# Optimization experiments

Hardware: AMD Instinct MI355X
Metric: run time of the kernel (lower is better)

The kernel has to match this reference:

```python
import jax, jax.numpy as jnp
import numpy as np

N_NODES = 100000
N_HEDGES = 50000
N_INC = 300000
N_GRAPHS = 1024
D_IN = 49
D = 512
L = 3
EPS = 1e-5


def _layernorm(x, g, b):
    mu = jnp.mean(x, axis=-1, keepdims=True)
    var = jnp.var(x, axis=-1, keepdims=True)
    return (x - mu) * jax.lax.rsqrt(var + EPS) * g + b


def setup_inputs() -> dict:
    key = jax.random.key(0)
    ks = jax.random.split(key, 20)
    s = 0.02
    inp = {
        "node_features": jax.random.normal(ks[0], (N_NODES, D_IN), jnp.float32),
        "node_idx": jax.random.randint(ks[1], (N_INC,), 0, N_NODES),
        "hedge_idx": jax.random.randint(ks[2], (N_INC,), 0, N_HEDGES),
        "hyperedge_types": jax.random.randint(ks[3], (N_HEDGES,), 0, 3),
        "batch_indices": jnp.sort(jax.random.randint(ks[4], (N_NODES,), 0, N_GRAPHS)),
        "num_graphs": N_GRAPHS,
        "in_w": jax.random.normal(ks[5], (D_IN, D), jnp.float32) * s,
        "in_b": jnp.zeros((D,), jnp.float32),
        "type_emb": jax.random.normal(ks[6], (3, D), jnp.float32) * s,
        "l1_w": jax.random.normal(ks[7], (L, D, D), jnp.float32) * s,
        "l1_b": jnp.zeros((L, D), jnp.float32),
        "l2_w": jax.random.normal(ks[8], (L, D, D), jnp.float32) * s,
        "l2_b": jnp.zeros((L, D), jnp.float32),
        "ln_g": jnp.ones((L, D), jnp.float32),
        "ln_b": jnp.zeros((L, D), jnp.float32),
        "out_w": jax.random.normal(ks[9], (D, D), jnp.float32) * s,
        "out_b": jnp.zeros((D,), jnp.float32),
    }
    return inp


def reference(node_features, node_idx, hedge_idx, hyperedge_types, batch_indices,
              num_graphs, in_w, in_b, type_emb, l1_w, l1_b, l2_w, l2_b,
              ln_g, ln_b, out_w, out_b):
    n_nodes = node_features.shape[0]
    n_hedges = hyperedge_types.shape[0]
    ones_e = jnp.ones((node_idx.shape[0],), node_features.dtype)
    # degrees are constant across layers
    hedge_deg = jnp.clip(jax.ops.segment_sum(ones_e, hedge_idx, num_segments=n_hedges), 1.0)[:, None]
    node_deg = jnp.clip(jax.ops.segment_sum(ones_e, node_idx, num_segments=n_nodes), 1.0)[:, None]

    x = node_features @ in_w + in_b  # [N, D]
    for i in range(L):
        x_trans = x @ l1_w[i] + l1_b[i]                                        # [N, D]
        hedge_aggr = jax.ops.segment_sum(x_trans[node_idx], hedge_idx,
                                         num_segments=n_hedges)                # [H, D]
        hedge_msg = hedge_aggr / hedge_deg + type_emb[hyperedge_types]         # [H, D]
        node_aggr = jax.ops.segment_sum(hedge_msg[hedge_idx], node_idx,
                                        num_segments=n_nodes) / node_deg       # [N, D]
        out = node_aggr @ l2_w[i] + l2_b[i]
        out = x + out  # in_dim == out_dim -> residual
        x = jax.nn.gelu(_layernorm(out, ln_g[i], ln_b[i]), approximate=False)

    node_embs = x
    graph_sum = jax.ops.segment_sum(x, batch_indices, num_segments=num_graphs)  # [B, D]
    counts = jnp.clip(jax.ops.segment_sum(jnp.ones((n_nodes,), x.dtype),
                                          batch_indices, num_segments=num_graphs), 1.0)[:, None]
    graph_emb = (graph_sum / counts) @ out_w + out_b
    return graph_emb, node_embs, batch_indices
```

## Files before the change

### kernel.cpp

```cpp
#include <hip/hip_runtime.h>
#include <math.h>

#define N_NODES  100000
#define N_HEDGES 50000
#define HPAD     50176
#define N_INC    300000
#define N_GRAPHS 1024
#define D_IN     49
#define D        512
#define NPAD     100096
#define KPAD_IN  64

typedef __attribute__((ext_vector_type(8))) short short8;
typedef __attribute__((ext_vector_type(8))) __bf16 bf16x8;
typedef __attribute__((ext_vector_type(4))) float f32x4;

__device__ __forceinline__ short f2bf(float f) {
    union { float f; unsigned u; } v; v.f = f;
    unsigned r = v.u + 0x7fffu + ((v.u >> 16) & 1u);
    return (short)(r >> 16);
}
__device__ __forceinline__ float bf2f(short s) {
    union { unsigned u; float f; } v; v.u = ((unsigned)(unsigned short)s) << 16;
    return v.f;
}

__device__ __forceinline__ float fast_gelu(float y) {
    const float y2 = y * y;
    const float p  = fmaf(y2, 0.0356774081f, 0.7978845608f);
    float arg = y * p * 2.8853900818f;
    arg = fminf(fmaxf(arg, -30.0f), 30.0f);
    const float u = __builtin_exp2f(arg);
    return y * u * __builtin_amdgcn_rcpf(1.0f + u);
}

__device__ __forceinline__ void gld16(const void* g, void* l) {
    __builtin_amdgcn_global_load_lds(
        (const __attribute__((address_space(1))) unsigned int*)g,
        (__attribute__((address_space(3))) unsigned int*)l, 16, 0, 0);
}

__global__ __launch_bounds__(512) void gemm_bf16(
    const short* __restrict__ A, const short* __restrict__ Bt,
    const float* __restrict__ bias,
    short* __restrict__ Cbf, float* __restrict__ Cf, short* __restrict__ CbfT, int strideT,
    const int* __restrict__ hcnt, const int* __restrict__ htypes,
    const float* __restrict__ tembW2, const float* __restrict__ bb,
    int K, int nby, int layerWGs, long aStr, long bStr, long cStr)
{
    __shared__ short lds[24576];
    const int tid  = threadIdx.x;
    const int lane = tid & 63;
    const int wave = tid >> 6;
    const int wr = wave >> 1;
    const int wc = wave & 1;

    const int nwg = gridDim.x;
    const int q8 = nwg >> 3, r8 = nwg & 7;
    const int xcd = blockIdx.x & 7, loc = blockIdx.x >> 3;
    int wg = (xcd < r8) ? (xcd * (q8 + 1) + loc) : (r8 * (q8 + 1) + (xcd - r8) * q8 + loc);
    if (layerWGs) {
        const int layer = wg / layerWGs;
        wg %= layerWGs;
        A += layer * aStr;
        Bt += layer * bStr;
        if (CbfT) CbfT += layer * cStr;
    }
    const long row0 = (long)(wg / nby) * 256;
    const int  col0 = (wg % nby) * 128;

    f32x4 acc[4][4];
    #pragma unroll
    for (int m = 0; m < 4; m++)
        #pragma unroll
        for (int n = 0; n < 4; n++)
            acc[m][n] = (f32x4)(0.0f);

    const int ch   = lane & 3;
    const int rofs = lane >> 2;
    const short* aSrc[2];
    const short* bSrc;
    #pragma unroll
    for (int j = 0; j < 2; j++) {
        const int rloc = (wave * 2 + j) * 16 + rofs;
        const int sw = (rloc >> 1) & 3;
        aSrc[j] = A + (row0 + rloc) * (long)K + (ch ^ sw) * 8;
    }
    {
        const int rlb = wave * 16 + rofs;
        const int swb = (rlb >> 1) & 3;
        bSrc = Bt + ((long)col0 + rlb) * K + (ch ^ swb) * 8;
    }

    const int ks = lane >> 4;
    const int rl = lane & 15;
    const int nk = K >> 5;

    gld16(aSrc[0], &lds[(wave * 2) * 16 * 32]);
    gld16(aSrc[1], &lds[(wave * 2 + 1) * 16 * 32]);
    gld16(bSrc,    &lds[16384 + wave * 16 * 32]);
    if (nk > 1) {
        gld16(aSrc[0] + 32, &lds[8192 + (wave * 2) * 16 * 32]);
        gld16(aSrc[1] + 32, &lds[8192 + (wave * 2 + 1) * 16 * 32]);
        gld16(bSrc    + 32, &lds[16384 + 4096 + wave * 16 * 32]);
    }

    for (int t = 0; t < nk; t++) {
        if (t + 1 < nk) asm volatile("s_waitcnt vmcnt(3)" ::: "memory");
        else            asm volatile("s_waitcnt vmcnt(0)" ::: "memory");
        __builtin_amdgcn_s_barrier();
        __builtin_amdgcn_sched_barrier(0);
        const int cb = t & 1;
        bf16x8 a[4], b[4];
        #pragma unroll
        for (int m = 0; m < 4; m++) {
            const int rr = wr * 64 + m * 16 + rl;
            a[m] = *(const bf16x8*)&lds[cb * 8192 + rr * 32 + (ks ^ ((rr >> 1) & 3)) * 8];
        }
        #pragma unroll
        for (int n = 0; n < 4; n++) {
            const int rr = wc * 64 + n * 16 + rl;
            b[n] = *(const bf16x8*)&lds[16384 + cb * 4096 + rr * 32 + (ks ^ ((rr >> 1) & 3)) * 8];
        }
        #pragma unroll
        for (int m = 0; m < 4; m++)
            #pragma unroll
            for (int n = 0; n < 4; n++)
                acc[m][n] = __builtin_amdgcn_mfma_f32_16x16x32_bf16(a[m], b[n], acc[m][n], 0, 0, 0);
        __builtin_amdgcn_sched_barrier(0);
        __builtin_amdgcn_s_barrier();
        if (t + 2 < nk) {
            gld16(aSrc[0] + (t + 2) * 32, &lds[cb * 8192 + (wave * 2) * 16 * 32]);
            gld16(aSrc[1] + (t + 2) * 32, &lds[cb * 8192 + (wave * 2 + 1) * 16 * 32]);
            gld16(bSrc    + (t + 2) * 32, &lds[16384 + cb * 4096 + wave * 16 * 32]);
        }
    }

    const int rl2 = lane & 15;
    if (Cbf && !Cf && !CbfT) {
        float bbv[4], tw0[4], tw1[4], tw2[4], biv[4];
        #pragma unroll
        for (int n = 0; n < 4; n++) {
            const int col = col0 + wc * 64 + n * 16 + rl2;
            if (hcnt) {
                bbv[n] = bb[col];
                tw0[n] = tembW2[col];
                tw1[n] = tembW2[D + col];
                tw2[n] = tembW2[2 * D + col];
            } else {
                biv[n] = bias ? bias[col] : 0.0f;
            }
        }
        short* ep = &lds[wave * 2304];
        #pragma unroll
        for (int p = 0; p < 2; p++) {
            #pragma unroll
            for (int mm = 0; mm < 2; mm++) {
                const int m = 2 * p + mm;
                #pragma unroll
                for (int rr = 0; rr < 4; rr++) {
                    const long row = row0 + wr * 64 + m * 16 + (lane >> 4) * 4 + rr;
                    const int  lr  = mm * 16 + (lane >> 4) * 4 + rr;
                    if (hcnt) {
                        const float cf  = (float)hcnt[row];
                        const float icf = 1.0f / fmaxf(cf, 1.0f);
                        const int ty = (row < N_HEDGES) ? htypes[row] : 0;
                        #pragma unroll
                        for (int n = 0; n < 4; n++) {
                            float tsel = (ty == 0) ? tw0[n] : (ty == 1) ? tw1[n] : tw2[n];
                            float v = (acc[m][n][rr] + cf * bbv[n]) * icf + tsel;
                            ep[lr * 72 + n * 16 + rl2] = f2bf(v);
                        }
                    } else {
                        #pragma unroll
                        for (int n = 0; n < 4; n++) {
                            float v = acc[m][n][rr] + biv[n];
                            ep[lr * 72 + n * 16 + rl2] = f2bf(v);
                        }
                    }
                }
            }
            __syncthreads();
            #pragma unroll
            for (int i = 0; i < 4; i++) {
                const int lr2 = i * 8 + (lane >> 3);
                const int c2  = lane & 7;
                short8 vv = *(const short8*)&ep[lr2 * 72 + c2 * 8];
                const long row = row0 + wr * 64 + p * 32 + lr2;
                *(short8*)&Cbf[row * D + col0 + wc * 64 + c2 * 8] = vv;
            }
            __syncthreads();
        }
    } else {
        const int rb4 = wr * 64 + (lane >> 4) * 4;
        #pragma unroll
        for (int m = 0; m < 4; m++) {
            #pragma unroll
            for (int n = 0; n < 4; n++) {
                const int col = col0 + wc * 64 + n * 16 + rl2;
                const float bi = bias ? bias[col] : 0.0f;
                #pragma unroll
                for (int rr = 0; rr < 4; rr++) {
                    const long row = row0 + rb4 + m * 16 + rr;
                    float v = acc[m][n][rr];
                    if (hcnt) {
                        const float cf = (float)hcnt[row];
                        const int ty = (row < N_HEDGES) ? htypes[row] : 0;
                        v = (v + cf * bb[col]) * (1.0f / fmaxf(cf, 1.0f)) + tembW2[(long)ty * D + col];
                    } else {
                        v += bi;
                    }
                    if (Cbf)  Cbf[row * D + col] = f2bf(v);
                    if (Cf)   Cf[row * D + col]  = v;
                    if (CbfT && row < strideT) CbfT[(long)col * strideT + row] = f2bf(v);
                }
            }
        }
    }
}

__global__ void count_inc_kernel(const int* __restrict__ nidx, const int* __restrict__ hidx,
                                 int* cnt_n, int* cnt_h) {
    int i = blockIdx.x * 256 + threadIdx.x;
    if (i < N_INC) {
        atomicAdd(&cnt_h[hidx[i]], 1);
        atomicAdd(&cnt_n[nidx[i]], 1);
    }
}

__global__ __launch_bounds__(256) void scan1_kernel(const int* __restrict__ cnt, int* __restrict__ out,
                                                    int* __restrict__ bsum, int n) {
    __shared__ int s[256];
    const int t = threadIdx.x;
    const long base = (long)blockIdx.x * 2048 + t * 8;
    int v[8];
    int ts = 0;
    #pragma unroll
    for (int j = 0; j < 8; j++) {
        v[j] = (base + j < n) ? cnt[base + j] : 0;
        ts += v[j];
    }
    s[t] = ts;
    __syncthreads();
    for (int ofs = 1; ofs < 256; ofs <<= 1) {
        int x = (t >= ofs) ? s[t - ofs] : 0;
        __syncthreads();
        s[t] += x;
        __syncthreads();
    }
    int run = (t == 0) ? 0 : s[t - 1];
    #pragma unroll
    for (int j = 0; j < 8; j++) {
        if (base + j < n) out[base + j] = run;
        run += v[j];
    }
    if (t == 255) bsum[blockIdx.x] = s[255];
}

__global__ __launch_bounds__(256) void scan2_kernel(int* __restrict__ bsum, int nb, int* __restrict__ total) {
    __shared__ int s[256];
    const int t = threadIdx.x;
    int v = (t < nb) ? bsum[t] : 0;
    s[t] = v;
    __syncthreads();
    for (int ofs = 1; ofs < 256; ofs <<= 1) {
        int x = (t >= ofs) ? s[t - ofs] : 0;
        __syncthreads();
        s[t] += x;
        __syncthreads();
    }
    if (t < nb) bsum[t] = (t == 0) ? 0 : s[t - 1];
    if (t == 255) *total = s[255];
}

__global__ __launch_bounds__(256) void scan3_kernel(int* __restrict__ out, const int* __restrict__ bsum, int n) {
    const int add = bsum[blockIdx.x];
    if (add == 0) return;
    const long base = (long)blockIdx.x * 2048 + threadIdx.x * 8;
    #pragma unroll
    for (int j = 0; j < 8; j++)
        if (base + j < n) out[base + j] += add;
}

__global__ void place_kernel(const int* __restrict__ nidx, const int* __restrict__ hidx,
                             const int* __restrict__ hoff, const int* __restrict__ noff,
                             int* hcur, int* ncur, int* __restrict__ hlist, int* __restrict__ nlist) {
    int e = blockIdx.x * 256 + threadIdx.x;
    if (e < N_INC) {
        int h = hidx[e], n = nidx[e];
        int p = atomicAdd(&hcur[h], 1);
        hlist[hoff[h] + p] = n;
        int q = atomicAdd(&ncur[n], 1);
        nlist[noff[n] + q] = h;
    }
}

__global__ void wtrans_kernel(const float* __restrict__ W, short* __restrict__ Wt, int K, int Kpad) {
    int n = blockIdx.x;
    for (int k = threadIdx.x; k < Kpad; k += 64)
        Wt[(long)n * Kpad + k] = (k < K) ? f2bf(W[(long)k * D + n]) : (short)0;
}

__global__ void wtrans3_kernel(const float* __restrict__ W, short* __restrict__ Wt) {
    int layer = blockIdx.x >> 9;
    int n = blockIdx.x & 511;
    const float* src = W + (size_t)layer * D * D;
    short* dst = Wt + (size_t)layer * D * D;
    for (int k = threadIdx.x; k < D; k += 64)
        dst[(long)n * D + k] = f2bf(src[(long)k * D + n]);
}

__global__ void cvt_f32_bf16_kernel(const float* __restrict__ src, short* __restrict__ dst) {
    long i = ((long)blockIdx.x * 256 + threadIdx.x) * 8;
    float4 f0 = *(const float4*)(src + i);
    float4 f1 = *(const float4*)(src + i + 4);
    short8 o;
    o[0] = f2bf(f0.x); o[1] = f2bf(f0.y); o[2] = f2bf(f0.z); o[3] = f2bf(f0.w);
    o[4] = f2bf(f1.x); o[5] = f2bf(f1.y); o[6] = f2bf(f1.z); o[7] = f2bf(f1.w);
    *(short8*)(dst + i) = o;
}

__global__ void cvt_w_pad_kernel(const float* __restrict__ src, short* __restrict__ dst, int rows_real) {
    int r = blockIdx.x;
    int c = threadIdx.x * 8;
    short8 o = (short8)0;
    if (r < rows_real) {
        float4 f0 = *(const float4*)(src + (long)r * D + c);
        float4 f1 = *(const float4*)(src + (long)r * D + c + 4);
        o[0] = f2bf(f0.x); o[1] = f2bf(f0.y); o[2] = f2bf(f0.z); o[3] = f2bf(f0.w);
        o[4] = f2bf(f1.x); o[5] = f2bf(f1.y); o[6] = f2bf(f1.z); o[7] = f2bf(f1.w);
    }
    *(short8*)(dst + (long)r * D + c) = o;
}

__global__ __launch_bounds__(256) void vecmat_kernel(const float* __restrict__ v,
                                                     const float* __restrict__ M,
                                                     float* __restrict__ out) {
    int col = blockIdx.x * 256 + threadIdx.x;
    float a = 0.f;
    for (int j = 0; j < D; j++) a += v[j] * M[(long)j * D + col];
    out[col] = a;
}

__global__ void vecadd_kernel(const float* __restrict__ a, const float* __restrict__ b,
                              float* __restrict__ o) {
    int i = blockIdx.x * 256 + threadIdx.x;
    o[i] = a[i] + b[i];
}

__global__ __launch_bounds__(256) void smallmm3_kernel(
    const float* __restrict__ temb, const float* __restrict__ l1b,
    const float* __restrict__ l2w, float* __restrict__ TB)
{
    int layer = blockIdx.x >> 1;
    int col = (blockIdx.x & 1) * 256 + threadIdx.x;
    const float* b1 = l1b + (size_t)layer * D;
    const float* W2 = l2w + (size_t)layer * D * D;
    float a0 = 0.f, a1 = 0.f, a2 = 0.f, a3 = 0.f;
    for (int j = 0; j < D; j++) {
        float w = W2[(long)j * D + col];
        a0 += temb[j] * w;
        a1 += temb[D + j] * w;
        a2 += temb[2 * D + j] * w;
        a3 += b1[j] * w;
    }
    float* o = TB + (size_t)layer * 4 * D;
    o[col] = a0; o[D + col] = a1; o[2 * D + col] = a2; o[3 * D + col] = a3;
}

__global__ void cvt_in_kernel(const float* __restrict__ nf, short* __restrict__ A0) {
    int r = blockIdx.x;
    int c = threadIdx.x;
    short v = 0;
    if (r < N_NODES && c < D_IN) v = f2bf(nf[(long)r * D_IN + c]);
    A0[(long)r * KPAD_IN + c] = v;
}

__global__ __launch_bounds__(256) void hedge_sum_kernel(
    const short* __restrict__ x, const int* __restrict__ hoff, const int* __restrict__ hlist,
    short* __restrict__ hs)
{
    int row = blockIdx.x * 4 + (threadIdx.x >> 6);
    int lane = threadIdx.x & 63;
    float acc[8] = {0, 0, 0, 0, 0, 0, 0, 0};
    if (row < N_HEDGES) {
        int s = hoff[row], e = hoff[row + 1];
        int j = s;
        for (; j + 1 < e; j += 2) {
            short8 v0 = *(const short8*)(x + (long)hlist[j] * D + lane * 8);
            short8 v1 = *(const short8*)(x + (long)hlist[j + 1] * D + lane * 8);
            #pragma unroll
            for (int k = 0; k < 8; k++) acc[k] += bf2f(v0[k]) + bf2f(v1[k]);
        }
        if (j < e) {
            short8 v0 = *(const short8*)(x + (long)hlist[j] * D + lane * 8);
            #pragma unroll
            for (int k = 0; k < 8; k++) acc[k] += bf2f(v0[k]);
        }
    }
    short8 o;
    #pragma unroll
    for (int k = 0; k < 8; k++) o[k] = f2bf(acc[k]);
    *(short8*)(hs + (long)row * D + lane * 8) = o;
}

__global__ __launch_bounds__(256) void hedge_sum64_kernel(
    const short* __restrict__ A0, const int* __restrict__ hoff, const int* __restrict__ hlist,
    short* __restrict__ hs0)
{
    int row = blockIdx.x * 4 + (threadIdx.x >> 6);
    int c = threadIdx.x & 63;
    float acc = 0.f;
    if (row < N_HEDGES) {
        int s = hoff[row], e = hoff[row + 1];
        int j = s;
        for (; j + 1 < e; j += 2) {
            float a = bf2f(A0[(long)hlist[j] * KPAD_IN + c]);
            float b = bf2f(A0[(long)hlist[j + 1] * KPAD_IN + c]);
            acc += a + b;
        }
        if (j < e) acc += bf2f(A0[(long)hlist[j] * KPAD_IN + c]);
    }
    hs0[(long)row * KPAD_IN + c] = f2bf(acc);
}

__global__ __launch_bounds__(256) void node_ln_gelu_kernel(
    const short* __restrict__ hmsg, const int* __restrict__ noff, const int* __restrict__ nlist,
    short* __restrict__ x, const float* __restrict__ b2,
    const float* __restrict__ g, const float* __restrict__ b, float* __restrict__ outf)
{
    const int row = blockIdx.x * 4 + (threadIdx.x >> 6);
    const int lane = threadIdx.x & 63;
    int s = noff[row], e = noff[row + 1];
    float acc[8] = {0, 0, 0, 0, 0, 0, 0, 0};
    int j = s;
    for (; j + 1 < e; j += 2) {
        short8 v0 = *(const short8*)(hmsg + (long)nlist[j] * D + lane * 8);
        short8 v1 = *(const short8*)(hmsg + (long)nlist[j + 1] * D + lane * 8);
        #pragma unroll
        for (int k = 0; k < 8; k++) acc[k] += bf2f(v0[k]) + bf2f(v1[k]);
    }
    if (j < e) {
        short8 v0 = *(const short8*)(hmsg + (long)nlist[j] * D + lane * 8);
        #pragma unroll
        for (int k = 0; k < 8; k++) acc[k] += bf2f(v0[k]);
    }
    const float inv = 1.0f / fmaxf((float)(e - s), 1.0f);
    short8 xv = *(const short8*)(x + (long)row * D + lane * 8);
    const float4 c0 = *(const float4*)(b2 + lane * 8);
    const float4 c1 = *(const float4*)(b2 + lane * 8 + 4);
    const float cv[8] = {c0.x, c0.y, c0.z, c0.w, c1.x, c1.y, c1.z, c1.w};
    float f[8];
    float sum = 0.f, sq = 0.f;
    #pragma unroll
    for (int k = 0; k < 8; k++) {
        f[k] = acc[k] * inv + bf2f(xv[k]) + cv[k];
        sum += f[k]; sq += f[k] * f[k];
    }
    #pragma unroll
    for (int o = 32; o > 0; o >>= 1) { sum += __shfl_xor(sum, o, 64); sq += __shfl_xor(sq, o, 64); }
    const float mean = sum * (1.0f / D);
    const float var  = sq * (1.0f / D) - mean * mean;
    const float rstd = rsqrtf(var + 1e-5f);
    const float4 g0 = *(const float4*)(g + lane * 8);
    const float4 g1 = *(const float4*)(g + lane * 8 + 4);
    const float4 b0 = *(const float4*)(b + lane * 8);
    const float4 b1 = *(const float4*)(b + lane * 8 + 4);
    const float gv[8] = {g0.x, g0.y, g0.z, g0.w, g1.x, g1.y, g1.z, g1.w};
    const float bv[8] = {b0.x, b0.y, b0.z, b0.w, b1.x, b1.y, b1.z, b1.w};
    float yout[8];
    #pragma unroll
    for (int k = 0; k < 8; k++) {
        float y = (f[k] - mean) * rstd * gv[k] + bv[k];
        yout[k] = fast_gelu(y);
    }
    if (outf) {
        float4 o0 = {yout[0], yout[1], yout[2], yout[3]};
        float4 o1 = {yout[4], yout[5], yout[6], yout[7]};
        *(float4*)(outf + (long)row * D + lane * 8) = o0;
        *(float4*)(outf + (long)row * D + lane * 8 + 4) = o1;
    } else {
        short8 o8;
        #pragma unroll
        for (int k = 0; k < 8; k++) o8[k] = f2bf(yout[k]);
        *(short8*)(x + (long)row * D + lane * 8) = o8;
    }
}

__global__ __launch_bounds__(64) void pool_kernel(const float* __restrict__ x, const int* __restrict__ batch,
                                                  short* __restrict__ Gbf) {
    int g = blockIdx.x;
    int lo = 0, hi = N_NODES;
    while (lo < hi) { int mid = (lo + hi) >> 1; if (batch[mid] < g) lo = mid + 1; else hi = mid; }
    int s = lo;
    hi = N_NODES;
    while (lo < hi) { int mid = (lo + hi) >> 1; if (batch[mid] < g + 1) lo = mid + 1; else hi = mid; }
    int e = lo;
    int lane = threadIdx.x;
    float acc[8] = {0, 0, 0, 0, 0, 0, 0, 0};
    for (int r = s; r < e; r++) {
        const float* rp = x + (long)r * D + lane * 8;
        float4 v0 = *(const float4*)rp;
        float4 v1 = *(const float4*)(rp + 4);
        acc[0] += v0.x; acc[1] += v0.y; acc[2] += v0.z; acc[3] += v0.w;
        acc[4] += v1.x; acc[5] += v1.y; acc[6] += v1.z; acc[7] += v1.w;
    }
    float inv = 1.0f / fmaxf((float)(e - s), 1.0f);
    short8 o;
    #pragma unroll
    for (int k = 0; k < 8; k++) o[k] = f2bf(acc[k] * inv);
    *(short8*)(Gbf + (long)g * D + lane * 8) = o;
}

__global__ void batchf_kernel(const int* __restrict__ batch, float* __restrict__ ob) {
    int i = blockIdx.x * 256 + threadIdx.x;
    if (i < N_NODES) ob[i] = (float)batch[i];
}

extern "C" void kernel_launch(void* const* d_in, const int* in_sizes, int n_in,
                              void* d_out, int out_size, void* d_ws, size_t ws_size,
                              hipStream_t stream) {
    (void)in_sizes; (void)n_in; (void)out_size; (void)ws_size;
    const float* nf    = (const float*)d_in[0];
    const int*   nidx  = (const int*)d_in[1];
    const int*   hidx  = (const int*)d_in[2];
    const int*   htype = (const int*)d_in[3];
    const int*   batch = (const int*)d_in[4];
    const float* in_w  = (const float*)d_in[6];
    const float* in_b  = (const float*)d_in[7];
    const float* temb  = (const float*)d_in[8];
    const float* l1w   = (const float*)d_in[9];
    const float* l1b   = (const float*)d_in[10];
    const float* l2w   = (const float*)d_in[11];
    const float* l2b   = (const float*)d_in[12];
    const float* lng   = (const float*)d_in[13];
    const float* lnb   = (const float*)d_in[14];
    const float* outw  = (const float*)d_in[15];
    const float* outb  = (const float*)d_in[16];

    float* out_graph = (float*)d_out;
    float* out_nodes = out_graph + (long)N_GRAPHS * D;
    float* out_batch = out_nodes + (long)N_NODES * D;

    char* wsb = (char*)d_ws;
    size_t off = 0;
    auto alloc = [&](size_t bytes) {
        void* p = wsb + off;
        off += (bytes + 255) & ~(size_t)255;
        return p;
    };
    short* x_bf  = (short*)alloc((size_t)NPAD * D * 2);
    short* hs_bf = (short*)alloc((size_t)HPAD * D * 2);
    short* h_bf  = (short*)alloc((size_t)HPAD * D * 2);
    short* hs0   = (short*)alloc((size_t)HPAD * KPAD_IN * 2);
    short* G_bf  = (short*)alloc((size_t)N_GRAPHS * D * 2);
    short* A0    = (short*)alloc((size_t)NPAD * KPAD_IN * 2);
    short* wt    = (short*)alloc((size_t)D * D * 2);
    short* wt3   = (short*)alloc((size_t)3 * D * D * 2);
    short* w1bf  = (short*)alloc((size_t)3 * D * D * 2);
    short* W12t  = (short*)alloc((size_t)3 * D * D * 2);
    short* inwbf = (short*)alloc((size_t)256 * D * 2);
    short* M0t   = (short*)alloc((size_t)D * KPAD_IN * 2);
    float* TB    = (float*)alloc((size_t)3 * 4 * D * 4);
    float* tmpv  = (float*)alloc((size_t)D * 4);
    float* bias0 = (float*)alloc((size_t)D * 4);
    float* bb0   = (float*)alloc((size_t)D * 4);
    int* cnt_h   = (int*)alloc((size_t)HPAD * 4);
    int* cnt_n   = (int*)alloc((size_t)N_NODES * 4);
    int* hoff    = (int*)alloc((size_t)(N_HEDGES + 1) * 4);
    int* noff    = (int*)alloc((size_t)(N_NODES + 1) * 4);
    int* hcur    = (int*)alloc((size_t)N_HEDGES * 4);
    int* ncur    = (int*)alloc((size_t)N_NODES * 4);
    int* hlist   = (int*)alloc((size_t)N_INC * 4);
    int* nlist   = (int*)alloc((size_t)N_INC * 4);
    int* bsum    = (int*)alloc((size_t)256 * 4);

    hipMemsetAsync(cnt_h, 0, (size_t)HPAD * 4, stream);
    hipMemsetAsync(cnt_n, 0, (size_t)N_NODES * 4, stream);
    hipMemsetAsync(hcur,  0, (size_t)N_HEDGES * 4, stream);
    hipMemsetAsync(ncur,  0, (size_t)N_NODES * 4, stream);
    count_inc_kernel<<<(N_INC + 255) / 256, 256, 0, stream>>>(nidx, hidx, cnt_n, cnt_h);
    const int NBH = (N_HEDGES + 2047) / 2048;
    const int NBN = (N_NODES + 2047) / 2048;
    scan1_kernel<<<NBH, 256, 0, stream>>>(cnt_h, hoff, bsum, N_HEDGES);
    scan2_kernel<<<1, 256, 0, stream>>>(bsum, NBH, hoff + N_HEDGES);
    scan3_kernel<<<NBH, 256, 0, stream>>>(hoff, bsum, N_HEDGES);
    scan1_kernel<<<NBN, 256, 0, stream>>>(cnt_n, noff, bsum, N_NODES);
    scan2_kernel<<<1, 256, 0, stream>>>(bsum, NBN, noff + N_NODES);
    scan3_kernel<<<NBN, 256, 0, stream>>>(noff, bsum, N_NODES);
    place_kernel<<<(N_INC + 255) / 256, 256, 0, stream>>>(nidx, hidx, hoff, noff, hcur, ncur, hlist, nlist);
    batchf_kernel<<<(N_NODES + 255) / 256, 256, 0, stream>>>(batch, out_batch);

    cvt_f32_bf16_kernel<<<(3 * D * D / 8) / 256, 256, 0, stream>>>(l1w, w1bf);
    wtrans3_kernel<<<3 * D, 64, 0, stream>>>(l2w, wt3);
    gemm_bf16<<<24, 512, 0, stream>>>(w1bf, wt3, nullptr, nullptr, nullptr, W12t, D,
                                      nullptr, nullptr, nullptr, nullptr, D, 4,
                                      8, (long)D * D, (long)D * D, (long)D * D);
    smallmm3_kernel<<<6, 256, 0, stream>>>(temb, l1b, l2w, TB);

    cvt_w_pad_kernel<<<256, 64, 0, stream>>>(in_w, inwbf, D_IN);
    gemm_bf16<<<4, 512, 0, stream>>>(inwbf, W12t, nullptr, nullptr, nullptr, M0t, KPAD_IN,
                                     nullptr, nullptr, nullptr, nullptr, D, 4, 0, 0, 0, 0);
    vecmat_kernel<<<2, 256, 0, stream>>>(in_b, l1w, tmpv);
    vecmat_kernel<<<2, 256, 0, stream>>>(tmpv, l2w, bias0);
    vecadd_kernel<<<2, 256, 0, stream>>>(bias0, TB + 3 * D, bb0);

    wtrans_kernel<<<D, 64, 0, stream>>>(in_w, wt, D_IN, KPAD_IN);
    cvt_in_kernel<<<NPAD, 64, 0, stream>>>(nf, A0);
    const int NWG  = (NPAD / 256) * 4;
    const int NWGH = (HPAD / 256) * 4;
    gemm_bf16<<<NWG, 512, 0, stream>>>(A0, wt, in_b, x_bf, nullptr, nullptr, 0,
                                       nullptr, nullptr, nullptr, nullptr, KPAD_IN, 4, 0, 0, 0, 0);

    for (int i = 0; i < 3; i++) {
        if (i == 0) {
            hedge_sum64_kernel<<<HPAD / 4, 256, 0, stream>>>(A0, hoff, hlist, hs0);
            gemm_bf16<<<NWGH, 512, 0, stream>>>(hs0, M0t, nullptr, h_bf, nullptr, nullptr, 0,
                                                cnt_h, htype, TB, bb0, KPAD_IN, 4, 0, 0, 0, 0);
        } else {
            hedge_sum_kernel<<<HPAD / 4, 256, 0, stream>>>(x_bf, hoff, hlist, hs_bf);
            gemm_bf16<<<NWGH, 512, 0, stream>>>(hs_bf, W12t + (size_t)i * D * D, nullptr,
                                                h_bf, nullptr, nullptr, 0,
                                                cnt_h, htype, TB + (size_t)i * 4 * D,
                                                TB + (size_t)i * 4 * D + 3 * D, D, 4, 0, 0, 0, 0);
        }
        node_ln_gelu_kernel<<<N_NODES / 4, 256, 0, stream>>>(h_bf, noff, nlist, x_bf,
                                                             l2b + (size_t)i * D,
                                                             lng + (size_t)i * D, lnb + (size_t)i * D,
                                                             (i < 2) ? nullptr : out_nodes);
    }

    pool_kernel<<<N_GRAPHS, 64, 0, stream>>>(out_nodes, batch, G_bf);
    wtrans_kernel<<<D, 64, 0, stream>>>(outw, wt, D, D);
    gemm_bf16<<<(N_GRAPHS / 256) * 4, 512, 0, stream>>>(G_bf, wt, outb, nullptr, out_graph, nullptr, 0,
                                                        nullptr, nullptr, nullptr, nullptr, D, 4, 0, 0, 0, 0);
}
```

Before: 887.0 us.

## Fuse small setup kernels, reuse counters for placement, parallelize pooling across waves

Several small preprocessing launches are merged. The batch float conversion moves into count_inc, the two scan2 launches become one two-block kernel, and vecmat plus vecadd are fused. Placement decrements the count arrays with atomicSub instead of using separate cursor arrays, which removes two memsets. The GEMM epilogue therefore reads hedge degrees from offset differences instead of the consumed counts. Pooling now uses four waves per graph with an LDS reduction, aiming to cut launch overhead and the serial per-graph loop.

```diff
diff --git a/kernel.cpp b/kernel.cpp
--- a/kernel.cpp
+++ b/kernel.cpp
@@ -44,7 +44,7 @@
     const short* __restrict__ A, const short* __restrict__ Bt,
     const float* __restrict__ bias,
     short* __restrict__ Cbf, float* __restrict__ Cf, short* __restrict__ CbfT, int strideT,
-    const int* __restrict__ hcnt, const int* __restrict__ htypes,
+    const int* __restrict__ hoffp, const int* __restrict__ htypes,
     const float* __restrict__ tembW2, const float* __restrict__ bb,
     int K, int nby, int layerWGs, long aStr, long bStr, long cStr)
 {
@@ -142,7 +142,7 @@
         #pragma unroll
         for (int n = 0; n < 4; n++) {
             const int col = col0 + wc * 64 + n * 16 + rl2;
-            if (hcnt) {
+            if (hoffp) {
                 bbv[n] = bb[col];
                 tw0[n] = tembW2[col];
                 tw1[n] = tembW2[D + col];
@@ -161,10 +161,11 @@
                 for (int rr = 0; rr < 4; rr++) {
                     const long row = row0 + wr * 64 + m * 16 + (lane >> 4) * 4 + rr;
                     const int  lr  = mm * 16 + (lane >> 4) * 4 + rr;
-                    if (hcnt) {
-                        const float cf  = (float)hcnt[row];
+                    if (hoffp) {
+                        const bool valid = row < N_HEDGES;
+                        const float cf  = valid ? (float)(hoffp[row + 1] - hoffp[row]) : 0.0f;
                         const float icf = 1.0f / fmaxf(cf, 1.0f);
-                        const int ty = (row < N_HEDGES) ? htypes[row] : 0;
+                        const int ty = valid ? htypes[row] : 0;
                         #pragma unroll
                         for (int n = 0; n < 4; n++) {
                             float tsel = (ty == 0) ? tw0[n] : (ty == 1) ? tw1[n] : tw2[n];
@@ -203,9 +204,10 @@
                 for (int rr = 0; rr < 4; rr++) {
                     const long row = row0 + rb4 + m * 16 + rr;
                     float v = acc[m][n][rr];
-                    if (hcnt) {
-                        const float cf = (float)hcnt[row];
-                        const int ty = (row < N_HEDGES) ? htypes[row] : 0;
+                    if (hoffp) {
+                        const bool valid = row < N_HEDGES;
+                        const float cf = valid ? (float)(hoffp[row + 1] - hoffp[row]) : 0.0f;
+                        const int ty = valid ? htypes[row] : 0;
                         v = (v + cf * bb[col]) * (1.0f / fmaxf(cf, 1.0f)) + tembW2[(long)ty * D + col];
                     } else {
                         v += bi;
@@ -220,12 +222,14 @@
 }
 
 __global__ void count_inc_kernel(const int* __restrict__ nidx, const int* __restrict__ hidx,
-                                 int* cnt_n, int* cnt_h) {
+                                 const int* __restrict__ batch, int* cnt_n, int* cnt_h,
+                                 float* __restrict__ ob) {
     int i = blockIdx.x * 256 + threadIdx.x;
     if (i < N_INC) {
         atomicAdd(&cnt_h[hidx[i]], 1);
         atomicAdd(&cnt_n[nidx[i]], 1);
     }
+    if (i < N_NODES) ob[i] = (float)batch[i];
 }
 
 __global__ __launch_bounds__(256) void scan1_kernel(const int* __restrict__ cnt, int* __restrict__ out,
@@ -257,7 +261,11 @@
     if (t == 255) bsum[blockIdx.x] = s[255];
 }
 
-__global__ __launch_bounds__(256) void scan2_kernel(int* __restrict__ bsum, int nb, int* __restrict__ total) {
+__global__ __launch_bounds__(256) void scan2both_kernel(int* __restrict__ bsumA, int nA, int* __restrict__ totalA,
+                                                        int* __restrict__ bsumB, int nB, int* __restrict__ totalB) {
+    int* bsum = blockIdx.x ? bsumB : bsumA;
+    int  nb   = blockIdx.x ? nB : nA;
+    int* total = blockIdx.x ? totalB : totalA;
     __shared__ int s[256];
     const int t = threadIdx.x;
     int v = (t < nb) ? bsum[t] : 0;
@@ -284,13 +292,13 @@
 
 __global__ void place_kernel(const int* __restrict__ nidx, const int* __restrict__ hidx,
                              const int* __restrict__ hoff, const int* __restrict__ noff,
-                             int* hcur, int* ncur, int* __restrict__ hlist, int* __restrict__ nlist) {
+                             int* cnt_h, int* cnt_n, int* __restrict__ hlist, int* __restrict__ nlist) {
     int e = blockIdx.x * 256 + threadIdx.x;
     if (e < N_INC) {
         int h = hidx[e], n = nidx[e];
-        int p = atomicAdd(&hcur[h], 1);
+        int p = atomicSub(&cnt_h[h], 1) - 1;
         hlist[hoff[h] + p] = n;
-        int q = atomicAdd(&ncur[n], 1);
+        int q = atomicSub(&cnt_n[n], 1) - 1;
         nlist[noff[n] + q] = h;
     }
 }
@@ -342,10 +350,14 @@
     out[col] = a;
 }
 
-__global__ void vecadd_kernel(const float* __restrict__ a, const float* __restrict__ b,
-                              float* __restrict__ o) {
-    int i = blockIdx.x * 256 + threadIdx.x;
-    o[i] = a[i] + b[i];
+__global__ __launch_bounds__(256) void vecmat_add_kernel(const float* __restrict__ v,
+                                                         const float* __restrict__ M,
+                                                         const float* __restrict__ addv,
+                                                         float* __restrict__ out) {
+    int col = blockIdx.x * 256 + threadIdx.x;
+    float a = addv[col];
+    for (int j = 0; j < D; j++) a += v[j] * M[(long)j * D + col];
+    out[col] = a;
 }
 
 __global__ __launch_bounds__(256) void smallmm3_kernel(
@@ -487,8 +499,8 @@
     }
 }
 
-__global__ __launch_bounds__(64) void pool_kernel(const float* __restrict__ x, const int* __restrict__ batch,
-                                                  short* __restrict__ Gbf) {
+__global__ __launch_bounds__(256) void pool_kernel(const float* __restrict__ x, const int* __restrict__ batch,
+                                                   short* __restrict__ Gbf) {
     int g = blockIdx.x;
     int lo = 0, hi = N_NODES;
     while (lo < hi) { int mid = (lo + hi) >> 1; if (batch[mid] < g) lo = mid + 1; else hi = mid; }
@@ -496,25 +508,31 @@
     hi = N_NODES;
     while (lo < hi) { int mid = (lo + hi) >> 1; if (batch[mid] < g + 1) lo = mid + 1; else hi = mid; }
     int e = lo;
-    int lane = threadIdx.x;
+    const int wv = threadIdx.x >> 6;
+    const int lane = threadIdx.x & 63;
     float acc[8] = {0, 0, 0, 0, 0, 0, 0, 0};
-    for (int r = s; r < e; r++) {
+    for (int r = s + wv; r < e; r += 4) {
         const float* rp = x + (long)r * D + lane * 8;
         float4 v0 = *(const float4*)rp;
         float4 v1 = *(const float4*)(rp + 4);
         acc[0] += v0.x; acc[1] += v0.y; acc[2] += v0.z; acc[3] += v0.w;
         acc[4] += v1.x; acc[5] += v1.y; acc[6] += v1.z; acc[7] += v1.w;
     }
-    float inv = 1.0f / fmaxf((float)(e - s), 1.0f);
-    short8 o;
-    #pragma unroll
-    for (int k = 0; k < 8; k++) o[k] = f2bf(acc[k] * inv);
-    *(short8*)(Gbf + (long)g * D + lane * 8) = o;
-}
-
-__global__ void batchf_kernel(const int* __restrict__ batch, float* __restrict__ ob) {
-    int i = blockIdx.x * 256 + threadIdx.x;
-    if (i < N_NODES) ob[i] = (float)batch[i];
+    __shared__ float red[4][512];
+    #pragma unroll
+    for (int k = 0; k < 8; k++) red[wv][lane * 8 + k] = acc[k];
+    __syncthreads();
+    if (wv == 0) {
+        const float invc = 1.0f / fmaxf((float)(e - s), 1.0f);
+        short8 o;
+        #pragma unroll
+        for (int k = 0; k < 8; k++) {
+            float v = red[0][lane * 8 + k] + red[1][lane * 8 + k]
+                    + red[2][lane * 8 + k] + red[3][lane * 8 + k];
+            o[k] = f2bf(v * invc);
+        }
+        *(short8*)(Gbf + (long)g * D + lane * 8) = o;
+    }
 }
 
 extern "C" void kernel_launch(void* const* d_in, const int* in_sizes, int n_in,
@@ -563,33 +581,27 @@
     short* M0t   = (short*)alloc((size_t)D * KPAD_IN * 2);
     float* TB    = (float*)alloc((size_t)3 * 4 * D * 4);
     float* tmpv  = (float*)alloc((size_t)D * 4);
-    float* bias0 = (float*)alloc((size_t)D * 4);
     float* bb0   = (float*)alloc((size_t)D * 4);
-    int* cnt_h   = (int*)alloc((size_t)HPAD * 4);
+    int* cnt_h   = (int*)alloc((size_t)N_HEDGES * 4);
     int* cnt_n   = (int*)alloc((size_t)N_NODES * 4);
     int* hoff    = (int*)alloc((size_t)(N_HEDGES + 1) * 4);
     int* noff    = (int*)alloc((size_t)(N_NODES + 1) * 4);
-    int* hcur    = (int*)alloc((size_t)N_HEDGES * 4);
-    int* ncur    = (int*)alloc((size_t)N_NODES * 4);
     int* hlist   = (int*)alloc((size_t)N_INC * 4);
     int* nlist   = (int*)alloc((size_t)N_INC * 4);
-    int* bsum    = (int*)alloc((size_t)256 * 4);
-
-    hipMemsetAsync(cnt_h, 0, (size_t)HPAD * 4, stream);
+    int* bsumH   = (int*)alloc((size_t)256 * 4);
+    int* bsumN   = (int*)alloc((size_t)256 * 4);
+
+    hipMemsetAsync(cnt_h, 0, (size_t)N_HEDGES * 4, stream);
     hipMemsetAsync(cnt_n, 0, (size_t)N_NODES * 4, stream);
-    hipMemsetAsync(hcur,  0, (size_t)N_HEDGES * 4, stream);
-    hipMemsetAsync(ncur,  0, (size_t)N_NODES * 4, stream);
-    count_inc_kernel<<<(N_INC + 255) / 256, 256, 0, stream>>>(nidx, hidx, cnt_n, cnt_h);
+    count_inc_kernel<<<(N_INC + 255) / 256, 256, 0, stream>>>(nidx, hidx, batch, cnt_n, cnt_h, out_batch);
     const int NBH = (N_HEDGES + 2047) / 2048;
     const int NBN = (N_NODES + 2047) / 2048;
-    scan1_kernel<<<NBH, 256, 0, stream>>>(cnt_h, hoff, bsum, N_HEDGES);
-    scan2_kernel<<<1, 256, 0, stream>>>(bsum, NBH, hoff + N_HEDGES);
-    scan3_kernel<<<NBH, 256, 0, stream>>>(hoff, bsum, N_HEDGES);
-    scan1_kernel<<<NBN, 256, 0, stream>>>(cnt_n, noff, bsum, N_NODES);
-    scan2_kernel<<<1, 256, 0, stream>>>(bsum, NBN, noff + N_NODES);
-    scan3_kernel<<<NBN, 256, 0, stream>>>(noff, bsum, N_NODES);
-    place_kernel<<<(N_INC + 255) / 256, 256, 0, stream>>>(nidx, hidx, hoff, noff, hcur, ncur, hlist, nlist);
-    batchf_kernel<<<(N_NODES + 255) / 256, 256, 0, stream>>>(batch, out_batch);
+    scan1_kernel<<<NBH, 256, 0, stream>>>(cnt_h, hoff, bsumH, N_HEDGES);
+    scan1_kernel<<<NBN, 256, 0, stream>>>(cnt_n, noff, bsumN, N_NODES);
+    scan2both_kernel<<<2, 256, 0, stream>>>(bsumH, NBH, hoff + N_HEDGES, bsumN, NBN, noff + N_NODES);
+    scan3_kernel<<<NBH, 256, 0, stream>>>(hoff, bsumH, N_HEDGES);
+    scan3_kernel<<<NBN, 256, 0, stream>>>(noff, bsumN, N_NODES);
+    place_kernel<<<(N_INC + 255) / 256, 256, 0, stream>>>(nidx, hidx, hoff, noff, cnt_h, cnt_n, hlist, nlist);
 
     cvt_f32_bf16_kernel<<<(3 * D * D / 8) / 256, 256, 0, stream>>>(l1w, w1bf);
     wtrans3_kernel<<<3 * D, 64, 0, stream>>>(l2w, wt3);
@@ -602,8 +614,7 @@
     gemm_bf16<<<4, 512, 0, stream>>>(inwbf, W12t, nullptr, nullptr, nullptr, M0t, KPAD_IN,
                                      nullptr, nullptr, nullptr, nullptr, D, 4, 0, 0, 0, 0);
     vecmat_kernel<<<2, 256, 0, stream>>>(in_b, l1w, tmpv);
-    vecmat_kernel<<<2, 256, 0, stream>>>(tmpv, l2w, bias0);
-    vecadd_kernel<<<2, 256, 0, stream>>>(bias0, TB + 3 * D, bb0);
+    vecmat_add_kernel<<<2, 256, 0, stream>>>(tmpv, l2w, TB + 3 * D, bb0);
 
     wtrans_kernel<<<D, 64, 0, stream>>>(in_w, wt, D_IN, KPAD_IN);
     cvt_in_kernel<<<NPAD, 64, 0, stream>>>(nf, A0);
@@ -616,12 +627,12 @@
         if (i == 0) {
             hedge_sum64_kernel<<<HPAD / 4, 256, 0, stream>>>(A0, hoff, hlist, hs0);
             gemm_bf16<<<NWGH, 512, 0, stream>>>(hs0, M0t, nullptr, h_bf, nullptr, nullptr, 0,
-                                                cnt_h, htype, TB, bb0, KPAD_IN, 4, 0, 0, 0, 0);
+                                                hoff, htype, TB, bb0, KPAD_IN, 4, 0, 0, 0, 0);
         } else {
             hedge_sum_kernel<<<HPAD / 4, 256, 0, stream>>>(x_bf, hoff, hlist, hs_bf);
             gemm_bf16<<<NWGH, 512, 0, stream>>>(hs_bf, W12t + (size_t)i * D * D, nullptr,
                                                 h_bf, nullptr, nullptr, 0,
-                                                cnt_h, htype, TB + (size_t)i * 4 * D,
+                                                hoff, htype, TB + (size_t)i * 4 * D,
                                                 TB + (size_t)i * 4 * D + 3 * D, D, 4, 0, 0, 0, 0);
         }
         node_ln_gelu_kernel<<<N_NODES / 4, 256, 0, stream>>>(h_bf, noff, nlist, x_bf,
@@ -630,7 +641,7 @@
                                                              (i < 2) ? nullptr : out_nodes);
     }
 
-    pool_kernel<<<N_GRAPHS, 64, 0, stream>>>(out_nodes, batch, G_bf);
+    pool_kernel<<<N_GRAPHS, 256, 0, stream>>>(out_nodes, batch, G_bf);
     wtrans_kernel<<<D, 64, 0, stream>>>(outw, wt, D, D);
     gemm_bf16<<<(N_GRAPHS / 256) * 4, 512, 0, stream>>>(G_bf, wt, outb, nullptr, out_graph, nullptr, 0,
                                                         nullptr, nullptr, nullptr, nullptr, D, 4, 0, 0, 0, 0);
```

After: 849.2 us. 1.04x faster.
